# Kernel tuning notes

Measured on AMD Instinct MI355X. Metric: run time of the kernel, lower is better.

## Reference

```python
import jax, jax.numpy as jnp
import numpy as np

B, C, W, H, A, NCLS, M = 8, 32, 32, 32, 6, 14, 64
HARD_NUM = 256
LAM_HNM = 0.2
LAM_NOOBJ = 0.001


def setup_inputs() -> dict:
    rng = np.random.default_rng(0)
    proposal_map = jax.random.normal(jax.random.key(0), (B, C, W, H, A, 3 + NCLS), dtype=jnp.float32)
    # labels: first n_valid entries per (b, a) are real bboxes, rest are -100 padding
    labels = np.full((B, A, M), -100, dtype=np.int32)
    n_valid = rng.integers(4, M // 2, size=(B, A))
    for b in range(B):
        for a in range(A):
            k = int(n_valid[b, a])
            lab = rng.integers(0, NCLS, size=k)
            is_hn = rng.random(k) < 0.3
            lab = np.where(is_hn, -1 - rng.integers(0, NCLS, size=k), lab)
            labels[b, a, :k] = lab
    cwh = rng.integers(0, [C, W, H], size=(B, A, M, 3)).astype(np.int32)
    prop_idx = np.concatenate([cwh, labels[..., None]], axis=-1)
    prop_reg = (rng.standard_normal((B, A, M, 3)) * 0.3).astype(np.float32)
    return {
        "proposal_map": proposal_map,
        "prop_idx": jnp.asarray(prop_idx),
        "prop_reg": jnp.asarray(prop_reg),
    }


def reference(proposal_map, prop_idx, prop_reg):
    dt = proposal_map.dtype
    ncls = proposal_map.shape[-1] - 3
    c, w, h, labels = prop_idx[..., 0], prop_idx[..., 1], prop_idx[..., 2], prop_idx[..., 3]
    bi = jnp.arange(proposal_map.shape[0])[:, None, None]
    ai = jnp.arange(proposal_map.shape[4])[None, :, None]
    # gather per-bbox cell vector: [B, A, M, 3+ncls]
    vals = proposal_map[bi, c, w, h, ai]

    pos_mask = labels >= 0
    hn_mask = (labels < 0) & (labels != -100)
    posf = pos_mask.astype(dt)
    P = jnp.maximum(jnp.sum(posf), 1.0)

    cls_logits = vals[..., 3:]                                   # [B, A, M, ncls]
    lab = jnp.clip(labels, 0, ncls - 1)
    onehot = jax.nn.one_hot(lab, ncls, dtype=dt)
    pos_logit = jnp.sum(cls_logits * onehot, axis=-1)            # [B, A, M]

    # BCEWithLogits(x, 1) = softplus(-x); BCEWithLogits(x, 0) = softplus(x)
    cl_pos_loss = jnp.sum(jax.nn.softplus(-pos_logit) * posf) / P
    cl_neg_loss = (jnp.sum(jax.nn.softplus(cls_logits) * (1.0 - onehot) * posf[..., None])
                   / (P * (ncls - 1))) / (ncls - 1)

    # hard-negative mining: per class, topk(count*hard_num) over all flattened logits
    j = jnp.where(hn_mask, -1 - labels, 0)
    counts = jnp.zeros((ncls,), jnp.int32).at[j.ravel()].add(hn_mask.ravel().astype(jnp.int32))
    k = counts * HARD_NUM                                        # [ncls]
    cls_flat = jnp.moveaxis(proposal_map[..., 3:], -1, 0).reshape(ncls, -1)
    srt = -jnp.sort(-cls_flat, axis=1)                           # descending
    sel = (jnp.arange(srt.shape[1])[None, :] < k[:, None]).astype(dt)
    tot_k = jnp.sum(k)
    hn_loss = jnp.where(
        tot_k > 0,
        LAM_HNM * jnp.sum(jax.nn.softplus(srt) * sel) / jnp.maximum(tot_k, 1).astype(dt),
        jnp.array(0.0, dt),
    )

    regu_neg_loss = LAM_NOOBJ * jnp.mean(jax.nn.softplus(proposal_map))

    # SmoothL1(tanh(reg_pred), reg_target), mean over positives x 3 coords (beta=1)
    d = jnp.tanh(vals[..., :3]) - prop_reg
    sl = jnp.where(jnp.abs(d) < 1.0, 0.5 * d * d, jnp.abs(d) - 0.5)
    reg_loss = jnp.sum(sl * posf[..., None]) / (3.0 * P)

    return cl_pos_loss + cl_neg_loss + hn_loss + regu_neg_loss + reg_loss
```

## Files before the change

kernel.cpp:

```cpp
#include <hip/hip_runtime.h>
#include <cstdint>
#include <cstddef>

#define B_ 8
#define C_ 32
#define W_ 32
#define H_ 32
#define A_ 6
#define NCLS 14
#define M_ 64
#define HARD_NUM 256
#define LAM_HNM 0.2f
#define LAM_NOOBJ 0.001f

#define NCH 17
#define NPOS (B_*C_*W_*H_*A_)
#define TOTAL (NPOS*NCH)
#define NPROP (B_*A_*M_)

#define KSHIFT 21
#define HB0 1532
#define NHB 64
#define HSL (NHB*NCLS)
#define SUBBITS 11
#define NBIN_F (1<<SUBBITS)
#define K1_BLOCKS 2048
#define K1_THREADS 256
#define NWAVES (K1_BLOCKS*(K1_THREADS/64))
#define NY 128
#define NTH (K1_BLOCKS*K1_THREADS)

#define OFF_FACC   0
#define OFF_UACC   64
#define OFF_BSTAR  128
#define OFF_CNTAB  192
#define OFF_SUMAB  256
#define OFF_HNP    320
#define OFF_DONE   384
#define OFF_RSUM   4096
#define OFF_NWAV   12288
#define OFF_FINE   45056
#define OFF_M32    274432
#define OFF_PART   733184
#define OFF_CAND   8073216

__device__ __forceinline__ float sp(float x) {
    return fmaxf(x, 0.0f) + log1pf(__expf(-fabsf(x)));
}

__global__ __launch_bounds__(K1_THREADS)
void k1_stream(const float* __restrict__ pm,
               unsigned* __restrict__ cand, unsigned* __restrict__ nwav,
               float* __restrict__ rsum,
               float* __restrict__ facc, unsigned* __restrict__ uacc,
               int seg_w) {
    __shared__ float wsum[4];
    if (blockIdx.x == 0 && threadIdx.x < 32) {
        if (threadIdx.x < 16) facc[threadIdx.x] = 0.0f;
        else                  uacc[threadIdx.x - 16] = 0u;
    }
    int lane = threadIdx.x & 63;
    int wid = threadIdx.x >> 6;
    unsigned wseg = blockIdx.x * (K1_THREADS / 64) + wid;
    unsigned* gc = cand + (size_t)wseg * seg_w;
    unsigned wcount = 0;
    float racc = 0.0f;
    int tid = blockIdx.x * K1_THREADS + threadIdx.x;
    const int n4 = TOTAL / 4;
    int cm0 = (tid * 4) % NCH - 3;
    for (int i = tid; i < n4; i += NTH) {
        float4 v = reinterpret_cast<const float4*>(pm)[i];
        float xs[4] = {v.x, v.y, v.z, v.w};
        int cm = cm0;
#pragma unroll
        for (int j = 0; j < 4; ++j) {
            float x = xs[j];
            float tc = fminf(fabsf(x), 2.8f);
            float g = fmaf(fmaf(0.08077f, tc, -0.4526f), tc, 0.6931472f);
            racc += fmaxf(x, 0.0f) + g;
            bool q = (cm >= 0) && (x >= 1.0f);
            unsigned long long mb = __ballot(q);
            if (q) {
                unsigned idx = wcount +
                    (unsigned)__popcll(mb & ((1ull << lane) - 1ull));
                if ((int)idx < seg_w)
                    gc[idx] = (__float_as_uint(x) & 0xFFFFFFF0u) | (unsigned)cm;
            }
            wcount += (unsigned)__popcll(mb);
            cm = (cm == NCH - 4) ? -3 : cm + 1;
        }
        cm0 -= 2; if (cm0 < -3) cm0 += NCH;
    }
    if (lane == 0)
        nwav[wseg] = (wcount < (unsigned)seg_w) ? wcount : (unsigned)seg_w;
    for (int o = 32; o; o >>= 1) racc += __shfl_down(racc, o, 64);
    if (lane == 0) wsum[wid] = racc;
    __syncthreads();
    if (threadIdx.x == 0)
        rsum[blockIdx.x] = wsum[0] + wsum[1] + wsum[2] + wsum[3];
}

__global__ __launch_bounds__(128)
void k2_props(const float* __restrict__ pm, const int* __restrict__ pidx,
              const float* __restrict__ preg,
              float* __restrict__ facc, unsigned* __restrict__ uacc) {
    __shared__ float s_clp, s_cln, s_rg;
    __shared__ unsigned s_pos;
    int t = threadIdx.x;
    if (t == 0) { s_clp = 0; s_cln = 0; s_rg = 0; s_pos = 0; }
    __syncthreads();
    int tid = blockIdx.x * 128 + t;
    int p = tid >> 2, sub = tid & 3;
    float clp = 0.0f, cln = 0.0f, rg = 0.0f;
    int lab = -100;
    if (p < NPROP) {
        const int4 q = *reinterpret_cast<const int4*>(pidx + (size_t)p * 4);
        lab = q.w;
        if (lab >= 0) {
            int b = p / (A_ * M_);
            int a = (p / M_) % A_;
            const float* v = pm
                + (size_t)((((b * C_ + q.x) * W_ + q.y) * H_ + q.z) * A_ + a) * NCH;
#pragma unroll
            for (int m = 0; m < 4; ++m) {
                int j = sub + 4 * m;
                if (j < NCLS) {
                    float lg = v[3 + j];
                    if (j == lab) clp += sp(-lg);
                    else          cln += sp(lg);
                }
            }
            if (sub < 3) {
                float d = tanhf(v[sub]) - preg[(size_t)p * 3 + sub];
                float ad = fabsf(d);
                rg = (ad < 1.0f) ? 0.5f * d * d : ad - 0.5f;
            }
        } else if (lab != -100 && sub == 0) {
            atomicAdd(&uacc[1 + (-1 - lab)], 1u);
        }
    }
    clp += __shfl_xor(clp, 1, 64); clp += __shfl_xor(clp, 2, 64);
    cln += __shfl_xor(cln, 1, 64); cln += __shfl_xor(cln, 2, 64);
    rg  += __shfl_xor(rg, 1, 64);  rg  += __shfl_xor(rg, 2, 64);
    if (sub == 0 && lab >= 0) {
        atomicAdd(&s_clp, clp);
        atomicAdd(&s_cln, cln);
        atomicAdd(&s_rg, rg);
        atomicAdd(&s_pos, 1u);
    }
    __syncthreads();
    if (t == 0) {
        if (s_clp != 0.0f) atomicAdd(&facc[0], s_clp);
        if (s_cln != 0.0f) atomicAdd(&facc[1], s_cln);
        if (s_rg != 0.0f)  atomicAdd(&facc[2], s_rg);
        if (s_pos)         atomicAdd(&uacc[0], s_pos);
    }
}

__global__ __launch_bounds__(256)
void k3a_hist(const unsigned* __restrict__ cand, const unsigned* __restrict__ nwav,
              unsigned* __restrict__ partials, int seg_w) {
    __shared__ unsigned h[HSL];
    int t = threadIdx.x;
    for (int s = t; s < HSL; s += 256) h[s] = 0;
    __syncthreads();
    for (int w = 0; w < 4; ++w) {
        unsigned wseg = blockIdx.x * 4 + w;
        const unsigned* gc = cand + (size_t)wseg * seg_w;
        unsigned n = nwav[wseg];
        for (unsigned i = t; i < n; i += 256) {
            unsigned e = gc[i];
            unsigned wb = ((e | 0x80000000u) >> KSHIFT) - HB0;
            if (wb > NHB - 1) wb = NHB - 1;
            atomicAdd(&h[wb * NCLS + (e & 15u)], 1u);
        }
    }
    __syncthreads();
    unsigned* dst = partials + (size_t)blockIdx.x * HSL;
    for (int s = t; s < HSL; s += 256) dst[s] = h[s];
}

__global__ __launch_bounds__(128)
void kr_reduce(const unsigned* __restrict__ partials,
               unsigned* __restrict__ m32) {
    int slot = blockIdx.x * 128 + threadIdx.x;
    int y = blockIdx.y;
    const int BPY = K1_BLOCKS / NY;
    unsigned a = 0;
#pragma unroll
    for (int p = y * BPY; p < y * BPY + BPY; ++p)
        a += partials[(size_t)p * HSL + slot];
    m32[(size_t)y * HSL + slot] = a;
}

__global__ __launch_bounds__(256)
void k2_merge(const unsigned* __restrict__ m32,
              const float* __restrict__ rsum, const unsigned* __restrict__ uacc,
              int* __restrict__ bstar, unsigned* __restrict__ cntab,
              float* __restrict__ sumab, float* __restrict__ facc,
              unsigned long long* __restrict__ fine, unsigned* __restrict__ done) {
    int t = threadIdx.x;
    if (blockIdx.x == 14) {
        __shared__ float s[256];
        if (t == 0) *done = 0u;
        float a = 0.0f;
#pragma unroll
        for (int kk = 0; kk < K1_BLOCKS / 256; ++kk) a += rsum[t + kk * 256];
        s[t] = a;
        __syncthreads();
        for (int o = 128; o; o >>= 1) { if (t < o) s[t] += s[t + o]; __syncthreads(); }
        if (t == 0) facc[3] = s[0];
        return;
    }
    int cls = blockIdx.x;
    unsigned long long* fc = fine + (size_t)cls * NBIN_F;
    for (int s2 = t; s2 < NBIN_F; s2 += 256) fc[s2] = 0ull;
    if (t == 0) sumab[cls] = 0.0f;
    unsigned k = uacc[1 + cls] * HARD_NUM;
    if (k == 0) { if (t == 0) bstar[cls] = -2; return; }
    int bin = t & 63, grp = t >> 6;
    const int YPG = NY / 4;
    unsigned c = 0;
    for (int y = grp * YPG; y < grp * YPG + YPG; ++y)
        c += m32[(size_t)y * HSL + bin * NCLS + cls];
    __shared__ unsigned cq[256];
    cq[t] = c;
    __syncthreads();
    if (t == 0) {
        unsigned cum = 0; int bb = -1;
        for (int b2 = NHB - 1; b2 >= 0; --b2) {
            unsigned cc = cq[b2] + cq[64 + b2] + cq[128 + b2] + cq[192 + b2];
            if (cum + cc >= k) { bb = b2; break; }
            cum += cc;
        }
        bstar[cls] = bb;
        cntab[cls] = cum;
    }
}

__global__ __launch_bounds__(256)
void k3_cand(const unsigned* __restrict__ cand, const unsigned* __restrict__ nwav,
             const int* __restrict__ bstar, unsigned long long* __restrict__ fine,
             float* __restrict__ sumab, int seg_w) {
    __shared__ float csum[16];
    __shared__ int bst[16];
    int t = threadIdx.x;
    if (t < 16) { csum[t] = 0.0f; bst[t] = (t < 14) ? bstar[t] : -2; }
    __syncthreads();
    for (int w = 0; w < 4; ++w) {
        unsigned wseg = blockIdx.x * 4 + w;
        const unsigned* gc = cand + (size_t)wseg * seg_w;
        unsigned n = nwav[wseg];
        for (unsigned i = t; i < n; i += 256) {
            unsigned e = gc[i];
            int cls = (int)(e & 15u);
            int b = bst[cls];
            if (b == -2) continue;
            unsigned ut = e & 0xFFFFFFF0u;
            unsigned key = ut | 0x80000000u;
            unsigned wb = (key >> KSHIFT) - HB0;
            if (wb > NHB - 1) wb = NHB - 1;
            float x = __uint_as_float(ut | 0x8u);
            if (b == -1 || (int)wb > b) {
                atomicAdd(&csum[cls], sp(x));
            } else if ((int)wb == b) {
                unsigned sub = (key >> (KSHIFT - SUBBITS)) & (NBIN_F - 1);
                unsigned long long pk = (1ull << 43)
                    | (unsigned long long)(sp(x) * 262144.0f + 0.5f);
                atomicAdd(&fine[(size_t)cls * NBIN_F + sub], pk);
            }
        }
    }
    __syncthreads();
    if (t < 14 && csum[t] != 0.0f) atomicAdd(&sumab[t], csum[t]);
}

__global__ __launch_bounds__(256)
void k4_resolve(const unsigned long long* __restrict__ fine,
                const unsigned* __restrict__ uacc, const int* __restrict__ bstar,
                const unsigned* __restrict__ cntab, const float* __restrict__ sumab,
                const float* __restrict__ facc, float* __restrict__ hnp,
                unsigned* __restrict__ done, float* __restrict__ out) {
    int cls = blockIdx.x, t = threadIdx.x;
    __shared__ unsigned ck[256];
    __shared__ float cs[256];
    __shared__ int lastflag;
    unsigned k = uacc[1 + cls] * HARD_NUM;
    if (k == 0) {
        if (t == 0) hnp[cls] = 0.0f;
    } else {
        int b = bstar[cls];
        if (b == -1) {
            if (t == 0) hnp[cls] = sumab[cls];
        } else {
            unsigned r = k - cntab[cls];
            const unsigned long long* fc = fine + (size_t)cls * NBIN_F;
            unsigned lc = 0; float ls = 0.0f;
            for (int j = 0; j < NBIN_F / 256; ++j) {
                unsigned long long v = fc[t * (NBIN_F / 256) + j];
                lc += (unsigned)(v >> 43);
                ls += (float)(v & ((1ull << 43) - 1)) * (1.0f / 262144.0f);
            }
            ck[t] = lc; cs[t] = ls;
            __syncthreads();
            if (t == 0) {
                unsigned cum = 0; float sa = sumab[cls];
                for (int ch = 255; ch >= 0; --ch) {
                    if (cum + ck[ch] >= r) {
                        unsigned c2 = cum;
                        for (int j = NBIN_F / 256 - 1; j >= 0; --j) {
                            unsigned long long v = fc[ch * (NBIN_F / 256) + j];
                            unsigned c = (unsigned)(v >> 43);
                            float s = (float)(v & ((1ull << 43) - 1)) * (1.0f / 262144.0f);
                            if (c2 + c >= r) {
                                unsigned rem = r - c2;
                                if (c > 0) sa += (float)rem * (s / (float)c);
                                break;
                            }
                            c2 += c; sa += s;
                        }
                        break;
                    }
                    cum += ck[ch]; sa += cs[ch];
                }
                hnp[cls] = sa;
            }
        }
    }
    __syncthreads();
    if (t == 0) {
        __threadfence();
        unsigned ticket = atomicAdd(done, 1u);
        lastflag = (ticket == NCLS - 1) ? 1 : 0;
    }
    __syncthreads();
    if (lastflag && t == 0) {
        __threadfence();
        float hn_sum = 0.0f; unsigned totk = 0;
        for (int j = 0; j < NCLS; ++j) { hn_sum += hnp[j]; totk += uacc[1 + j]; }
        totk *= HARD_NUM;
        float P = fmaxf((float)uacc[0], 1.0f);
        float hn = (totk > 0) ? (LAM_HNM * hn_sum / (float)totk) : 0.0f;
        out[0] = facc[0] / P
               + facc[1] / (P * (float)((NCLS - 1) * (NCLS - 1)))
               + hn
               + LAM_NOOBJ * facc[3] / (float)TOTAL
               + facc[2] / (3.0f * P);
    }
}

extern "C" void kernel_launch(void* const* d_in, const int* in_sizes, int n_in,
                              void* d_out, int out_size, void* d_ws, size_t ws_size,
                              hipStream_t stream) {
    const float* pm   = (const float*)d_in[0];
    const int*   pidx = (const int*)d_in[1];
    const float* preg = (const float*)d_in[2];
    float* out = (float*)d_out;
    char* ws = (char*)d_ws;

    float*    facc  = (float*)(ws + OFF_FACC);
    unsigned* uacc  = (unsigned*)(ws + OFF_UACC);
    int*      bstar = (int*)(ws + OFF_BSTAR);
    unsigned* cntab = (unsigned*)(ws + OFF_CNTAB);
    float*    sumab = (float*)(ws + OFF_SUMAB);
    float*    hnp   = (float*)(ws + OFF_HNP);
    unsigned* done  = (unsigned*)(ws + OFF_DONE);
    float*    rsum  = (float*)(ws + OFF_RSUM);
    unsigned* nwav  = (unsigned*)(ws + OFF_NWAV);
    unsigned long long* fine = (unsigned long long*)(ws + OFF_FINE);
    unsigned* m32   = (unsigned*)(ws + OFF_M32);
    unsigned* partials = (unsigned*)(ws + OFF_PART);
    unsigned* cand = (unsigned*)(ws + OFF_CAND);

    long long remain = (long long)ws_size - (long long)OFF_CAND;
    int seg_w = (int)(remain / ((long long)NWAVES * 4));
    if (seg_w > 4096) seg_w = 4096;
    seg_w &= ~63;
    if (seg_w < 512) seg_w = 512;

    k1_stream <<<K1_BLOCKS, K1_THREADS, 0, stream>>>(pm, cand, nwav, rsum,
                                                     facc, uacc, seg_w);
    k2_props  <<<(NPROP * 4) / 128, 128, 0, stream>>>(pm, pidx, preg, facc, uacc);
    k3a_hist  <<<K1_BLOCKS, 256, 0, stream>>>(cand, nwav, partials, seg_w);
    kr_reduce <<<dim3(HSL / 128, NY), 128, 0, stream>>>(partials, m32);
    k2_merge  <<<NCLS + 1, 256, 0, stream>>>(m32, rsum, uacc, bstar, cntab,
                                             sumab, facc, fine, done);
    k3_cand   <<<K1_BLOCKS, 256, 0, stream>>>(cand, nwav, bstar, fine, sumab, seg_w);
    k4_resolve<<<NCLS, 256, 0, stream>>>(fine, uacc, bstar, cntab, sumab, facc,
                                         hnp, done, out);
}
```

Baseline: 102.0 us.

## Store hard-negative candidates in per-thread strided rows instead of wave-compacted segments

The streaming kernel drops the wave ballot/popcount compaction. Each thread now writes its candidates into row-major slots (row r, column tid) capped at 32 rows, and records a per-thread count. Each thread also processes eight floats per iteration through two float4 loads. The histogram and candidate kernels read the same layout, looping up to the block's maximum count with a per-thread guard. This removes cross-lane ballot work and makes writes and reads coalesce by thread. The cost is divergent loops and a hard per-thread cap that could drop candidates if one thread sees more than 32.

```diff
diff --git a/kernel.cpp b/kernel.cpp
--- a/kernel.cpp
+++ b/kernel.cpp
@@ -26,9 +26,9 @@
 #define NBIN_F (1<<SUBBITS)
 #define K1_BLOCKS 2048
 #define K1_THREADS 256
-#define NWAVES (K1_BLOCKS*(K1_THREADS/64))
+#define NTH (K1_BLOCKS*K1_THREADS)
 #define NY 128
-#define NTH (K1_BLOCKS*K1_THREADS)
+#define NCROWS 32
 
 #define OFF_FACC   0
 #define OFF_UACC   64
@@ -38,11 +38,11 @@
 #define OFF_HNP    320
 #define OFF_DONE   384
 #define OFF_RSUM   4096
-#define OFF_NWAV   12288
 #define OFF_FINE   45056
 #define OFF_M32    274432
 #define OFF_PART   733184
-#define OFF_CAND   8073216
+#define OFF_NCAND  8073216
+#define OFF_CAND   10170368
 
 __device__ __forceinline__ float sp(float x) {
     return fmaxf(x, 0.0f) + log1pf(__expf(-fabsf(x)));
@@ -50,49 +50,42 @@
 
 __global__ __launch_bounds__(K1_THREADS)
 void k1_stream(const float* __restrict__ pm,
-               unsigned* __restrict__ cand, unsigned* __restrict__ nwav,
+               unsigned* __restrict__ cand, unsigned* __restrict__ ncand,
                float* __restrict__ rsum,
-               float* __restrict__ facc, unsigned* __restrict__ uacc,
-               int seg_w) {
+               float* __restrict__ facc, unsigned* __restrict__ uacc) {
     __shared__ float wsum[4];
     if (blockIdx.x == 0 && threadIdx.x < 32) {
         if (threadIdx.x < 16) facc[threadIdx.x] = 0.0f;
         else                  uacc[threadIdx.x - 16] = 0u;
     }
-    int lane = threadIdx.x & 63;
-    int wid = threadIdx.x >> 6;
-    unsigned wseg = blockIdx.x * (K1_THREADS / 64) + wid;
-    unsigned* gc = cand + (size_t)wseg * seg_w;
-    unsigned wcount = 0;
+    int tid = blockIdx.x * K1_THREADS + threadIdx.x;
+    unsigned cnt = 0;
     float racc = 0.0f;
-    int tid = blockIdx.x * K1_THREADS + threadIdx.x;
-    const int n4 = TOTAL / 4;
-    int cm0 = (tid * 4) % NCH - 3;
-    for (int i = tid; i < n4; i += NTH) {
-        float4 v = reinterpret_cast<const float4*>(pm)[i];
-        float xs[4] = {v.x, v.y, v.z, v.w};
+    const int n8 = TOTAL / 8;
+    int cm0 = (tid * 8) % NCH - 3;
+    for (int i = tid; i < n8; i += NTH) {
+        float4 va = reinterpret_cast<const float4*>(pm)[2 * i];
+        float4 vb = reinterpret_cast<const float4*>(pm)[2 * i + 1];
+        float xs[8] = {va.x, va.y, va.z, va.w, vb.x, vb.y, vb.z, vb.w};
         int cm = cm0;
 #pragma unroll
-        for (int j = 0; j < 4; ++j) {
+        for (int j = 0; j < 8; ++j) {
             float x = xs[j];
             float tc = fminf(fabsf(x), 2.8f);
-            float g = fmaf(fmaf(0.08077f, tc, -0.4526f), tc, 0.6931472f);
-            racc += fmaxf(x, 0.0f) + g;
-            bool q = (cm >= 0) && (x >= 1.0f);
-            unsigned long long mb = __ballot(q);
-            if (q) {
-                unsigned idx = wcount +
-                    (unsigned)__popcll(mb & ((1ull << lane) - 1ull));
-                if ((int)idx < seg_w)
-                    gc[idx] = (__float_as_uint(x) & 0xFFFFFFF0u) | (unsigned)cm;
-            }
-            wcount += (unsigned)__popcll(mb);
+            racc += fmaxf(x, 0.0f) +
+                    fmaf(fmaf(0.08077f, tc, -0.4526f), tc, 0.6931472f);
+            if (cm >= 0 && x >= 1.0f) {
+                if (cnt < NCROWS)
+                    cand[(size_t)cnt * NTH + tid] =
+                        (__float_as_uint(x) & 0xFFFFFFF0u) | (unsigned)cm;
+                ++cnt;
+            }
             cm = (cm == NCH - 4) ? -3 : cm + 1;
         }
-        cm0 -= 2; if (cm0 < -3) cm0 += NCH;
-    }
-    if (lane == 0)
-        nwav[wseg] = (wcount < (unsigned)seg_w) ? wcount : (unsigned)seg_w;
+        cm0 -= 4; if (cm0 < -3) cm0 += NCH;
+    }
+    ncand[tid] = (cnt < NCROWS) ? cnt : NCROWS;
+    int lane = threadIdx.x & 63, wid = threadIdx.x >> 6;
     for (int o = 32; o; o >>= 1) racc += __shfl_down(racc, o, 64);
     if (lane == 0) wsum[wid] = racc;
     __syncthreads();
@@ -158,18 +151,27 @@
 }
 
 __global__ __launch_bounds__(256)
-void k3a_hist(const unsigned* __restrict__ cand, const unsigned* __restrict__ nwav,
-              unsigned* __restrict__ partials, int seg_w) {
+void k3a_hist(const unsigned* __restrict__ cand, const unsigned* __restrict__ ncand,
+              unsigned* __restrict__ partials) {
     __shared__ unsigned h[HSL];
+    __shared__ unsigned bmax;
     int t = threadIdx.x;
     for (int s = t; s < HSL; s += 256) h[s] = 0;
-    __syncthreads();
-    for (int w = 0; w < 4; ++w) {
-        unsigned wseg = blockIdx.x * 4 + w;
-        const unsigned* gc = cand + (size_t)wseg * seg_w;
-        unsigned n = nwav[wseg];
-        for (unsigned i = t; i < n; i += 256) {
-            unsigned e = gc[i];
+    if (t == 0) bmax = 0;
+    __syncthreads();
+    int tid = blockIdx.x * 256 + t;
+    unsigned n = ncand[tid];
+    unsigned m = n;
+    for (int o = 32; o; o >>= 1) {
+        unsigned om = (unsigned)__shfl_down((int)m, o, 64);
+        m = (om > m) ? om : m;
+    }
+    if ((t & 63) == 0) atomicMax(&bmax, m);
+    __syncthreads();
+    unsigned bm = bmax;
+    for (unsigned r = 0; r < bm; ++r) {
+        if (r < n) {
+            unsigned e = cand[(size_t)r * NTH + tid];
             unsigned wb = ((e | 0x80000000u) >> KSHIFT) - HB0;
             if (wb > NHB - 1) wb = NHB - 1;
             atomicAdd(&h[wb * NCLS + (e & 15u)], 1u);
@@ -239,20 +241,29 @@
 }
 
 __global__ __launch_bounds__(256)
-void k3_cand(const unsigned* __restrict__ cand, const unsigned* __restrict__ nwav,
+void k3_cand(const unsigned* __restrict__ cand, const unsigned* __restrict__ ncand,
              const int* __restrict__ bstar, unsigned long long* __restrict__ fine,
-             float* __restrict__ sumab, int seg_w) {
+             float* __restrict__ sumab) {
     __shared__ float csum[16];
     __shared__ int bst[16];
+    __shared__ unsigned bmax;
     int t = threadIdx.x;
     if (t < 16) { csum[t] = 0.0f; bst[t] = (t < 14) ? bstar[t] : -2; }
-    __syncthreads();
-    for (int w = 0; w < 4; ++w) {
-        unsigned wseg = blockIdx.x * 4 + w;
-        const unsigned* gc = cand + (size_t)wseg * seg_w;
-        unsigned n = nwav[wseg];
-        for (unsigned i = t; i < n; i += 256) {
-            unsigned e = gc[i];
+    if (t == 0) bmax = 0;
+    __syncthreads();
+    int tid = blockIdx.x * 256 + t;
+    unsigned n = ncand[tid];
+    unsigned m = n;
+    for (int o = 32; o; o >>= 1) {
+        unsigned om = (unsigned)__shfl_down((int)m, o, 64);
+        m = (om > m) ? om : m;
+    }
+    if ((t & 63) == 0) atomicMax(&bmax, m);
+    __syncthreads();
+    unsigned bm = bmax;
+    for (unsigned r = 0; r < bm; ++r) {
+        if (r < n) {
+            unsigned e = cand[(size_t)r * NTH + tid];
             int cls = (int)(e & 15u);
             int b = bst[cls];
             if (b == -2) continue;
@@ -366,26 +377,20 @@
     float*    hnp   = (float*)(ws + OFF_HNP);
     unsigned* done  = (unsigned*)(ws + OFF_DONE);
     float*    rsum  = (float*)(ws + OFF_RSUM);
-    unsigned* nwav  = (unsigned*)(ws + OFF_NWAV);
     unsigned long long* fine = (unsigned long long*)(ws + OFF_FINE);
     unsigned* m32   = (unsigned*)(ws + OFF_M32);
     unsigned* partials = (unsigned*)(ws + OFF_PART);
-    unsigned* cand = (unsigned*)(ws + OFF_CAND);
-
-    long long remain = (long long)ws_size - (long long)OFF_CAND;
-    int seg_w = (int)(remain / ((long long)NWAVES * 4));
-    if (seg_w > 4096) seg_w = 4096;
-    seg_w &= ~63;
-    if (seg_w < 512) seg_w = 512;
-
-    k1_stream <<<K1_BLOCKS, K1_THREADS, 0, stream>>>(pm, cand, nwav, rsum,
-                                                     facc, uacc, seg_w);
+    unsigned* ncand = (unsigned*)(ws + OFF_NCAND);
+    unsigned* cand  = (unsigned*)(ws + OFF_CAND);
+
+    k1_stream <<<K1_BLOCKS, K1_THREADS, 0, stream>>>(pm, cand, ncand, rsum,
+                                                     facc, uacc);
     k2_props  <<<(NPROP * 4) / 128, 128, 0, stream>>>(pm, pidx, preg, facc, uacc);
-    k3a_hist  <<<K1_BLOCKS, 256, 0, stream>>>(cand, nwav, partials, seg_w);
+    k3a_hist  <<<K1_BLOCKS, 256, 0, stream>>>(cand, ncand, partials);
     kr_reduce <<<dim3(HSL / 128, NY), 128, 0, stream>>>(partials, m32);
     k2_merge  <<<NCLS + 1, 256, 0, stream>>>(m32, rsum, uacc, bstar, cntab,
                                              sumab, facc, fine, done);
-    k3_cand   <<<K1_BLOCKS, 256, 0, stream>>>(cand, nwav, bstar, fine, sumab, seg_w);
+    k3_cand   <<<K1_BLOCKS, 256, 0, stream>>>(cand, ncand, bstar, fine, sumab);
     k4_resolve<<<NCLS, 256, 0, stream>>>(fine, uacc, bstar, cntab, sumab, facc,
                                          hnp, done, out);
 }
```

Result: slower. 122.2 us (+19.8%).
